# Optimization experiments

Measured on AMD Instinct MI355X. Metric: run time of the kernel, lower is better.

## Reference

```python
import jax, jax.numpy as jnp
import numpy as np

B, S, HID = 2, 2048, 2048
H, KV, D = 16, 4, 128          # query heads, kv heads, head_dim
G = H // KV                     # q heads per kv head
RD = 32                         # rotary_dim = int(0.25 * 128), even
THETA = 5000000.0
EPS = 1e-6


def _rms_norm(x, w):
    # out = x * rsqrt(mean(x^2)) * (1 + w)   (weight is zero-init)
    out = x * jax.lax.rsqrt(jnp.mean(x * x, axis=-1, keepdims=True) + EPS)
    return out * (1.0 + w.astype(x.dtype))


def _apply_rope(x, positions):
    # x: [B,S,h,RD]; standard HF rope with rotate_half on the rotary slice
    half = RD // 2
    inv_freq = 1.0 / (THETA ** (jnp.arange(0, half, dtype=jnp.float32) * 2.0 / RD))
    freqs = positions.astype(jnp.float32)[..., None] * inv_freq  # [B,S,half]
    emb = jnp.concatenate([freqs, freqs], axis=-1)               # [B,S,RD]
    cos = jnp.cos(emb)[:, :, None, :].astype(x.dtype)
    sin = jnp.sin(emb)[:, :, None, :].astype(x.dtype)
    x1, x2 = x[..., :half], x[..., half:]
    rot = jnp.concatenate([-x2, x1], axis=-1)
    return x * cos + rot * sin


def _partial_rope(q, k, positions):
    q_rot, q_pass = q[..., :RD], q[..., RD:]
    k_rot, k_pass = k[..., :RD], k[..., RD:]
    q_rot = _apply_rope(q_rot, positions)
    k_rot = _apply_rope(k_rot, positions)
    return (jnp.concatenate([q_rot, q_pass], axis=-1),
            jnp.concatenate([k_rot, k_pass], axis=-1))


def setup_inputs() -> dict:
    k0, k1, k2 = jax.random.split(jax.random.key(0), 3)
    x = jax.random.normal(k0, (B, S, HID), dtype=jnp.float32)
    positions = jnp.broadcast_to(jnp.arange(S, dtype=jnp.int32), (B, S))
    attention_mask = jnp.ones((B, S), dtype=bool)
    wqkv = jax.random.normal(k1, (HID, (H * 2 + 2 * KV) * D), dtype=jnp.float32) * 0.02
    wo = jax.random.normal(k2, (H * D, HID), dtype=jnp.float32) * 0.02
    q_norm_w = jnp.zeros((D,), dtype=jnp.float32)
    k_norm_w = jnp.zeros((D,), dtype=jnp.float32)
    return {"x": x, "positions": positions, "attention_mask": attention_mask,
            "wqkv": wqkv, "wo": wo, "q_norm_w": q_norm_w, "k_norm_w": k_norm_w}


def reference(x, positions, attention_mask, wqkv, wo, q_norm_w, k_norm_w):
    bsz, seq, _ = x.shape
    qkv = jnp.einsum('bsh,hf->bsf', x, wqkv)  # [B,S,5120]
    q_sz, kv_sz = H * 2 * D, KV * D
    q_raw = qkv[..., :q_sz]
    k_raw = qkv[..., q_sz:q_sz + kv_sz]
    v_raw = qkv[..., q_sz + kv_sz:]

    q_all = q_raw.reshape(bsz, seq, H, 2 * D)
    q, gate = jnp.split(q_all, 2, axis=-1)          # each [B,S,H,D]
    gate = gate.reshape(bsz, seq, H * D)

    q = _rms_norm(q, q_norm_w)
    k = _rms_norm(k_raw.reshape(bsz, seq, KV, D), k_norm_w)
    v = v_raw.reshape(bsz, seq, KV, D)
    q, k = _partial_rope(q, k, positions)

    # GQA causal attention, scale = 1/sqrt(head_dim)
    qg = q.reshape(bsz, seq, KV, G, D)
    scores = jnp.einsum('bqkgd,bskd->bkgqs', qg, k) * (1.0 / np.sqrt(D))
    causal = jnp.tril(jnp.ones((seq, seq), dtype=bool))
    mask = causal[None, None, None] & attention_mask[:, None, None, None, :]
    scores = jnp.where(mask, scores, jnp.finfo(scores.dtype).min)
    probs = jax.nn.softmax(scores, axis=-1)
    attn = jnp.einsum('bkgqs,bskd->bqkgd', probs, v)
    attn = attn.reshape(bsz, seq, H * D)

    attn = attn * jax.nn.sigmoid(gate)
    return jnp.einsum('bsf,fh->bsh', attn, wo)
```

## Files before the change

### kernel.cpp

```cpp
#include <hip/hip_runtime.h>

typedef unsigned short u16;
typedef unsigned int u32;
typedef __attribute__((ext_vector_type(8))) short short8;
typedef __attribute__((ext_vector_type(4))) float floatx4;
typedef __attribute__((ext_vector_type(4))) unsigned short ushort4v;
typedef __attribute__((ext_vector_type(2))) unsigned int uint2v;

#define SEQ   2048
#define HIDD  2048
#define NQH   16
#define NKV   4
#define HDIM  128
#define QKV_N 5120
#define K_OFF 4096
#define V_OFF 4608
#define NTOK  4096
#define PSTR  40

__device__ __forceinline__ float b2f(u16 u) {
  u32 x = ((u32)u) << 16;
  return __builtin_bit_cast(float, x);
}
__device__ __forceinline__ u16 f2b(float f) {
  u32 x = __builtin_bit_cast(u32, f);
  u32 r = x + 0x7fffu + ((x >> 16) & 1u);
  return (u16)(r >> 16);
}
__device__ __forceinline__ u32 cvt_pk_bf16(float lo, float hi) {
  u32 r;
  asm("v_cvt_pk_bf16_f32 %0, %1, %2" : "=v"(r) : "v"(lo), "v"(hi));
  return r;
}
__device__ __forceinline__ short8 pack8(floatx4 a, floatx4 b) {
  short8 s;
#pragma unroll
  for (int j = 0; j < 4; j++) { s[j] = (short)f2b(a[j]); s[4 + j] = (short)f2b(b[j]); }
  return s;
}
__device__ __forceinline__ void async_copy16(const u16* g, u16* lds) {
  __builtin_amdgcn_global_load_lds((const __attribute__((address_space(1))) u32*)g,
                                   (__attribute__((address_space(3))) u32*)lds, 16, 0, 0);
}

__global__ __launch_bounds__(256) void cast_bf16(const float* __restrict__ in,
                                                 u16* __restrict__ out, int n8) {
  const int i = blockIdx.x * 256 + threadIdx.x;
  if (i < n8) {
    const floatx4 f0 = *(const floatx4*)(in + (size_t)i * 8);
    const floatx4 f1 = *(const floatx4*)(in + (size_t)i * 8 + 4);
    *(short8*)(out + (size_t)i * 8) = pack8(f0, f1);
  }
}

__global__ __launch_bounds__(256) void transpose_f32_bf16(const float* __restrict__ in,
                                                          u16* __restrict__ out,
                                                          int R, int C) {
  __shared__ float tile[64][65];
  const int bx = blockIdx.x * 64;
  const int by = blockIdx.y * 64;
  const int tid = threadIdx.x;
  const int lr  = tid >> 2;
  const int lc4 = tid & 3;
#pragma unroll
  for (int i = 0; i < 4; i++) {
    const int c4 = lc4 * 4 + i;
    *(floatx4*)&tile[lr][c4 * 4] =
        *(const floatx4*)&in[(size_t)(by + lr) * C + bx + c4 * 4];
  }
  __syncthreads();
#pragma unroll
  for (int i = 0; i < 2; i++) {
    const int c  = (tid >> 3) + i * 32;
    const int r0 = (tid & 7) * 8;
    short8 v;
#pragma unroll
    for (int k = 0; k < 8; k++) v[k] = (short)f2b(tile[r0 + k][c]);
    *(short8*)&out[(size_t)(bx + c) * R + by + r0] = v;
  }
}

__global__ __launch_bounds__(256) void pack_kv(const u16* __restrict__ qkv,
                                               u16* __restrict__ Kc,
                                               u16* __restrict__ Vp) {
  __shared__ u16 tile[32][136];
  const int t0 = blockIdx.x * 32;
  const int kv = blockIdx.y;
  const int tid = threadIdx.x;
  const int b  = t0 / SEQ;
  const int tl = t0 - b * SEQ;
  const int jt = tl >> 5;
  const size_t kvbase = (size_t)(b * NKV + kv) * SEQ * HDIM;

  const int row  = tid >> 3;
  const int part = tid & 7;
  const size_t qbase = (size_t)(t0 + row) * QKV_N;
  const short8 kv0 = *(const short8*)(qkv + qbase + K_OFF + kv * HDIM + part * 16);
  const short8 kv1 = *(const short8*)(qkv + qbase + K_OFF + kv * HDIM + part * 16 + 8);
  *(short8*)(Kc + kvbase + (size_t)(tl + row) * HDIM + part * 16)     = kv0;
  *(short8*)(Kc + kvbase + (size_t)(tl + row) * HDIM + part * 16 + 8) = kv1;
  const short8 vv0 = *(const short8*)(qkv + qbase + V_OFF + kv * HDIM + part * 16);
  const short8 vv1 = *(const short8*)(qkv + qbase + V_OFF + kv * HDIM + part * 16 + 8);
  *(short8*)&tile[row][part * 16]     = vv0;
  *(short8*)&tile[row][part * 16 + 8] = vv1;
  __syncthreads();
  const int d = tid >> 1;
  const int half = tid & 1;
  u16* vout = Vp + kvbase + (size_t)jt * HDIM * 32 + d * 32 + half * 16;
  short8 o0;
#pragma unroll
  for (int i = 0; i < 8; i++) o0[i] = (short)tile[half * 16 + i][d];
  short8 o1;
#pragma unroll
  for (int i = 0; i < 8; i++) o1[i] = (short)tile[half * 16 + 8 + i][d];
  *(short8*)(vout) = o0;
  *(short8*)(vout + 8) = o1;
}

template <bool C32>
__global__ __launch_bounds__(512, 2) void gemm_bt8(const u16* __restrict__ A,
                                                   const u16* __restrict__ Bt,
                                                   void* __restrict__ Cp,
                                                   int M, int N, int K, int ldc) {
  __shared__ __align__(16) u16 As[2][256 * 64];
  __shared__ __align__(16) u16 Bs[2][256 * 64];
  const int tid  = threadIdx.x;
  const int wave = tid >> 6;
  const int lane = tid & 63;
  const int lm   = lane & 15;
  const int lq   = lane >> 4;
  const int nwg = gridDim.x * gridDim.y;
  const int bid = blockIdx.y * gridDim.x + blockIdx.x;
  const int sbid = (bid & 7) * (nwg >> 3) + (bid >> 3);
  const int m0   = (sbid / gridDim.x) * 256;
  const int n0   = (sbid % gridDim.x) * 256;
  const int wr   = wave >> 2;
  const int wc   = wave & 3;
  const int NK   = K >> 6;

  const int r0 = wave * 16 + (lane >> 3);
  const int c0 = (((lane & 7) ^ (r0 & 7)) << 3);
  const int dls = wave * 1024;

  auto stageA = [&](int buf, int kt, int h) {
    const u16* g = A + (size_t)(m0 + h * 128 + r0) * K + kt * 64 + c0;
    async_copy16(g,                &As[buf][h * 8192 + dls]);
    async_copy16(g + (size_t)8 * K, &As[buf][h * 8192 + dls + 512]);
  };
  auto stageB = [&](int buf, int kt, int h) {
    const u16* g = Bt + (size_t)(n0 + h * 128 + r0) * K + kt * 64 + c0;
    async_copy16(g,                &Bs[buf][h * 8192 + dls]);
    async_copy16(g + (size_t)8 * K, &Bs[buf][h * 8192 + dls + 512]);
  };
  auto rdA = [&](int buf, int row, int ch) {
    return *(const short8*)&As[buf][row * 64 + ((ch ^ (row & 7)) << 3)];
  };
  auto rdB = [&](int buf, int row, int ch) {
    return *(const short8*)&Bs[buf][row * 64 + ((ch ^ (row & 7)) << 3)];
  };

  floatx4 acc[8][4] = {};
  short8 aF[4][2], bF[4][2];

  stageA(0, 0, 0); stageA(0, 0, 1);
  stageB(0, 0, 0); stageB(0, 0, 1);
  stageB(1, 1, 0); stageB(1, 1, 1);
  asm volatile("s_waitcnt vmcnt(4)" ::: "memory");
  __builtin_amdgcn_sched_barrier(0);
  __builtin_amdgcn_s_barrier();

  for (int j = 0; j < NK; ++j) {
    const int cur = j & 1;
#pragma unroll
    for (int m = 0; m < 4; ++m)
#pragma unroll
      for (int kk = 0; kk < 2; ++kk)
        aF[m][kk] = rdA(cur, wr * 128 + m * 16 + lm, kk * 4 + lq);
#pragma unroll
    for (int n = 0; n < 2; ++n)
#pragma unroll
      for (int kk = 0; kk < 2; ++kk)
        bF[n][kk] = rdB(cur, wc * 64 + n * 16 + lm, kk * 4 + lq);
    if (j + 1 < NK) stageA(cur ^ 1, j + 1, 0);
    asm volatile("s_waitcnt lgkmcnt(8)" ::: "memory");
    __builtin_amdgcn_s_barrier();
    asm volatile("s_waitcnt lgkmcnt(0)" ::: "memory");
    __builtin_amdgcn_sched_barrier(0);
    __builtin_amdgcn_s_setprio(1);
#pragma unroll
    for (int m = 0; m < 4; ++m)
#pragma unroll
      for (int n = 0; n < 2; ++n)
#pragma unroll
        for (int kk = 0; kk < 2; ++kk)
          acc[m][n] = __builtin_amdgcn_mfma_f32_16x16x32_bf16(aF[m][kk], bF[n][kk], acc[m][n], 0, 0, 0);
    __builtin_amdgcn_s_setprio(0);
    __builtin_amdgcn_s_barrier();
#pragma unroll
    for (int n = 0; n < 2; ++n)
#pragma unroll
      for (int kk = 0; kk < 2; ++kk)
        bF[2 + n][kk] = rdB(cur, wc * 64 + (2 + n) * 16 + lm, kk * 4 + lq);
    if (j + 1 < NK) stageA(cur ^ 1, j + 1, 1);
    __builtin_amdgcn_s_barrier();
    asm volatile("s_waitcnt lgkmcnt(0)" ::: "memory");
    __builtin_amdgcn_sched_barrier(0);
    __builtin_amdgcn_s_setprio(1);
#pragma unroll
    for (int m = 0; m < 4; ++m)
#pragma unroll
      for (int n = 0; n < 2; ++n)
#pragma unroll
        for (int kk = 0; kk < 2; ++kk)
          acc[m][2 + n] = __builtin_amdgcn_mfma_f32_16x16x32_bf16(aF[m][kk], bF[2 + n][kk], acc[m][2 + n], 0, 0, 0);
    __builtin_amdgcn_s_setprio(0);
    __builtin_amdgcn_s_barrier();
#pragma unroll
    for (int m = 0; m < 4; ++m)
#pragma unroll
      for (int kk = 0; kk < 2; ++kk)
        aF[m][kk] = rdA(cur, wr * 128 + 64 + m * 16 + lm, kk * 4 + lq);
    if (j + 2 < NK) stageB(cur, j + 2, 0);
    __builtin_amdgcn_s_barrier();
    asm volatile("s_waitcnt lgkmcnt(0)" ::: "memory");
    __builtin_amdgcn_sched_barrier(0);
    __builtin_amdgcn_s_setprio(1);
#pragma unroll
    for (int m = 0; m < 4; ++m)
#pragma unroll
      for (int n = 0; n < 2; ++n)
#pragma unroll
        for (int kk = 0; kk < 2; ++kk)
          acc[4 + m][n] = __builtin_amdgcn_mfma_f32_16x16x32_bf16(aF[m][kk], bF[n][kk], acc[4 + m][n], 0, 0, 0);
    __builtin_amdgcn_s_setprio(0);
    __builtin_amdgcn_s_barrier();
    if (j + 2 < NK) stageB(cur, j + 2, 1);
    __builtin_amdgcn_s_barrier();
    __builtin_amdgcn_s_setprio(1);
#pragma unroll
    for (int m = 0; m < 4; ++m)
#pragma unroll
      for (int n = 0; n < 2; ++n)
#pragma unroll
        for (int kk = 0; kk < 2; ++kk)
          acc[4 + m][2 + n] = __builtin_amdgcn_mfma_f32_16x16x32_bf16(aF[m][kk], bF[2 + n][kk], acc[4 + m][2 + n], 0, 0, 0);
    __builtin_amdgcn_s_setprio(0);
    if (j + 2 < NK) asm volatile("s_waitcnt vmcnt(4)" ::: "memory");
    else            asm volatile("s_waitcnt vmcnt(0)" ::: "memory");
    __builtin_amdgcn_sched_barrier(0);
    __builtin_amdgcn_s_barrier();
  }

#pragma unroll
  for (int mi = 0; mi < 8; ++mi)
#pragma unroll
    for (int ni = 0; ni < 4; ++ni)
#pragma unroll
      for (int r = 0; r < 4; ++r) {
        const int row = m0 + wr * 128 + mi * 16 + lq * 4 + r;
        const int col = n0 + wc * 64 + ni * 16 + lm;
        if (C32) ((float*)Cp)[(size_t)row * ldc + col] = acc[mi][ni][r];
        else     ((u16*)Cp)[(size_t)row * ldc + col] = f2b(acc[mi][ni][r]);
      }
}

template <bool C32>
__global__ __launch_bounds__(256) void gemm_bt128(const u16* __restrict__ A,
                                                  const u16* __restrict__ Bt,
                                                  void* __restrict__ Cp,
                                                  int M, int N, int K, int ldc) {
  __shared__ __align__(16) u16 As[128 * 32];
  __shared__ __align__(16) u16 Bs[128 * 32];
  const int tid  = threadIdx.x;
  const int wave = tid >> 6;
  const int lane = tid & 63;
  const int m0 = blockIdx.y * 128;
  const int n0 = blockIdx.x * 128;
  const int wr = wave >> 1, wc = wave & 1;
  const int lrow = lane >> 2;
  const int lcol = (lane & 3) * 8;
  const int lm = lane & 15;
  const int lq = lane >> 4;

  floatx4 acc[4][4] = {};

  for (int k0 = 0; k0 < K; k0 += 32) {
#pragma unroll
    for (int i = 0; i < 2; i++) {
      const int r = wave * 32 + i * 16;
      async_copy16(A  + (size_t)(m0 + r + lrow) * K + k0 + lcol, &As[r * 32]);
      async_copy16(Bt + (size_t)(n0 + r + lrow) * K + k0 + lcol, &Bs[r * 32]);
    }
    __syncthreads();
    short8 aF[4], bF[4];
#pragma unroll
    for (int mi = 0; mi < 4; mi++)
      aF[mi] = *(const short8*)&As[(wr * 64 + mi * 16 + lm) * 32 + lq * 8];
#pragma unroll
    for (int ni = 0; ni < 4; ni++)
      bF[ni] = *(const short8*)&Bs[(wc * 64 + ni * 16 + lm) * 32 + lq * 8];
#pragma unroll
    for (int mi = 0; mi < 4; mi++)
#pragma unroll
      for (int ni = 0; ni < 4; ni++)
        acc[mi][ni] = __builtin_amdgcn_mfma_f32_16x16x32_bf16(aF[mi], bF[ni], acc[mi][ni], 0, 0, 0);
    __syncthreads();
  }

#pragma unroll
  for (int mi = 0; mi < 4; mi++)
#pragma unroll
    for (int ni = 0; ni < 4; ni++)
#pragma unroll
      for (int r = 0; r < 4; r++) {
        const int row = m0 + wr * 64 + mi * 16 + lq * 4 + r;
        const int col = n0 + wc * 64 + ni * 16 + lm;
        if (C32) ((float*)Cp)[(size_t)row * ldc + col] = acc[mi][ni][r];
        else     ((u16*)Cp)[(size_t)row * ldc + col] = f2b(acc[mi][ni][r]);
      }
}

template <bool C32>
__global__ __launch_bounds__(512, 2) void gemm_n128(const u16* __restrict__ A,
                                                    const u16* __restrict__ Bt,
                                                    void* __restrict__ Cp,
                                                    int M, int N, int K, int ldc) {
  __shared__ __align__(16) u16 As[2][256 * 64];
  __shared__ __align__(16) u16 Bs[2][128 * 64];
  const int tid  = threadIdx.x;
  const int wave = tid >> 6;
  const int lane = tid & 63;
  const int lm   = lane & 15;
  const int lq   = lane >> 4;
  const int nwg = gridDim.x * gridDim.y;
  const int bid = blockIdx.y * gridDim.x + blockIdx.x;
  const int sbid = (bid & 7) * (nwg >> 3) + (bid >> 3);
  const int m0   = (sbid / gridDim.x) * 256;
  const int n0   = (sbid % gridDim.x) * 128;
  const int wr   = wave >> 1;
  const int wc   = wave & 1;
  const int NK   = K >> 6;

  auto stA = [&](int buf, int kt, int L) {
    const int cd  = L * 512 + wave * 64 + lane;
    const int row = cd >> 3;
    const int ch  = cd & 7;
    async_copy16(A + (size_t)(m0 + row) * K + kt * 64 + ((ch ^ (row & 7)) << 3),
                 &As[buf][(L * 512 + wave * 64) * 8]);
  };
  auto stB = [&](int buf, int kt, int L) {
    const int cd  = L * 512 + wave * 64 + lane;
    const int row = cd >> 3;
    const int ch  = cd & 7;
    async_copy16(Bt + (size_t)(n0 + row) * K + kt * 64 + ((ch ^ (row & 7)) << 3),
                 &Bs[buf][(L * 512 + wave * 64) * 8]);
  };
  auto rdA = [&](int buf, int row, int ch) {
    return *(const short8*)&As[buf][row * 64 + ((ch ^ (row & 7)) << 3)];
  };
  auto rdB = [&](int buf, int row, int ch) {
    return *(const short8*)&Bs[buf][row * 64 + ((ch ^ (row & 7)) << 3)];
  };

  floatx4 acc[4][4] = {};
  short8 aF[4][2], bF[4][2];

  stA(0, 0, 0); stA(0, 0, 1); stA(0, 0, 2); stA(0, 0, 3);
  stB(0, 0, 0); stB(0, 0, 1);
  stB(1, 1, 0); stB(1, 1, 1);
  asm volatile("s_waitcnt vmcnt(2)" ::: "memory");
  __builtin_amdgcn_sched_barrier(0);
  __builtin_amdgcn_s_barrier();

  for (int j = 0; j < NK; ++j) {
    const int cur = j & 1;
#pragma unroll
    for (int m = 0; m < 4; ++m)
#pragma unroll
      for (int kk = 0; kk < 2; ++kk)
        aF[m][kk] = rdA(cur, wr * 64 + m * 16 + lm, kk * 4 + lq);
#pragma unroll
    for (int n = 0; n < 4; ++n)
#pragma unroll
      for (int kk = 0; kk < 2; ++kk)
        bF[n][kk] = rdB(cur, wc * 64 + n * 16 + lm, kk * 4 + lq);
    if (j + 1 < NK) { stA(cur ^ 1, j + 1, 0); stA(cur ^ 1, j + 1, 1); }
    asm volatile("s_waitcnt lgkmcnt(8)" ::: "memory");
    __builtin_amdgcn_s_barrier();
    asm volatile("s_waitcnt lgkmcnt(0)" ::: "memory");
    __builtin_amdgcn_sched_barrier(0);
    __builtin_amdgcn_s_setprio(1);
#pragma unroll
    for (int m = 0; m < 4; ++m)
#pragma unroll
      for (int n = 0; n < 2; ++n)
#pragma unroll
        for (int kk = 0; kk < 2; ++kk)
          acc[m][n] = __builtin_amdgcn_mfma_f32_16x16x32_bf16(aF[m][kk], bF[n][kk], acc[m][n], 0, 0, 0);
    __builtin_amdgcn_s_setprio(0);
    __builtin_amdgcn_s_barrier();
    if (j + 1 < NK) { stA(cur ^ 1, j + 1, 2); stA(cur ^ 1, j + 1, 3); }
    if (j + 2 < NK) { stB(cur, j + 2, 0); stB(cur, j + 2, 1); }
    __builtin_amdgcn_s_barrier();
    __builtin_amdgcn_sched_barrier(0);
    __builtin_amdgcn_s_setprio(1);
#pragma unroll
    for (int m = 0; m < 4; ++m)
#pragma unroll
      for (int n = 0; n < 2; ++n)
#pragma unroll
        for (int kk = 0; kk < 2; ++kk)
          acc[m][2 + n] = __builtin_amdgcn_mfma_f32_16x16x32_bf16(aF[m][kk], bF[2 + n][kk], acc[m][2 + n], 0, 0, 0);
    __builtin_amdgcn_s_setprio(0);
    if (j + 2 < NK) asm volatile("s_waitcnt vmcnt(2)" ::: "memory");
    else            asm volatile("s_waitcnt vmcnt(0)" ::: "memory");
    __builtin_amdgcn_sched_barrier(0);
    __builtin_amdgcn_s_barrier();
  }

#pragma unroll
  for (int mi = 0; mi < 4; ++mi)
#pragma unroll
    for (int ni = 0; ni < 4; ++ni)
#pragma unroll
      for (int r = 0; r < 4; ++r) {
        const int row = m0 + wr * 64 + mi * 16 + lq * 4 + r;
        const int col = n0 + wc * 64 + ni * 16 + lm;
        if (C32) ((float*)Cp)[(size_t)row * ldc + col] = acc[mi][ni][r];
        else     ((u16*)Cp)[(size_t)row * ldc + col] = f2b(acc[mi][ni][r]);
      }
}

__global__ __launch_bounds__(256) void postproc(u16* __restrict__ qkv,
                                                const int* __restrict__ positions,
                                                const float* __restrict__ qw,
                                                const float* __restrict__ kw) {
  const int u    = blockIdx.y;
  const int wv   = threadIdx.x >> 6;
  const int lane = threadIdx.x & 63;
  const float* w;
  int base;
  if (u < NQH) { base = u * 256; w = qw; }
  else         { base = K_OFF + (u - NQH) * HDIM; w = kw; }
  const int d0 = lane * 2;
  const float w0 = 1.0f + w[d0];
  const float w1 = 1.0f + w[d0 + 1];
  float inv0 = 0.0f, inv1 = 0.0f;
  if (d0 < 32) {
    const int i = d0 & 15;
    inv0 = __powf(5.0e6f, -((float)i) / 16.0f);
    inv1 = __powf(5.0e6f, -((float)(i + 1)) / 16.0f);
  }
  const float qsc = (u < NQH) ? 0.08838834764831845f : 1.0f;
#pragma unroll
  for (int it = 0; it < 4; ++it) {
    const int tok = blockIdx.x * 16 + wv * 4 + it;
    u16* p = qkv + (size_t)tok * QKV_N + base;
    float v0 = b2f(p[d0]);
    float v1 = b2f(p[d0 + 1]);
    float ss = v0 * v0 + v1 * v1;
#pragma unroll
    for (int off = 32; off >= 1; off >>= 1) ss += __shfl_xor(ss, off, 64);
    const float rs = rsqrtf(ss * (1.0f / 128.0f) + 1e-6f);
    v0 = v0 * rs * w0;
    v1 = v1 * rs * w1;
    const float pv0 = __shfl_xor(v0, 8, 64);
    const float pv1 = __shfl_xor(v1, 8, 64);
    if (d0 < 32) {
      const float fpos = (float)positions[tok];
      float s0, c0, s1, c1;
      __sincosf(fpos * inv0, &s0, &c0);
      __sincosf(fpos * inv1, &s1, &c1);
      if (d0 < 16) { v0 = v0 * c0 - pv0 * s0; v1 = v1 * c1 - pv1 * s1; }
      else         { v0 = v0 * c0 + pv0 * s0; v1 = v1 * c1 + pv1 * s1; }
    }
    p[d0]     = f2b(v0 * qsc);
    p[d0 + 1] = f2b(v1 * qsc);
  }
}

__global__ __launch_bounds__(256) void attn_kernel(const u16* __restrict__ qkv,
                                                   const u16* __restrict__ Kc,
                                                   const u16* __restrict__ Vp,
                                                   u16* __restrict__ attn_g) {
  __shared__ __align__(16) u16 Ks[2][4][32][32];
  __shared__ __align__(16) u16 Vs[2][128][32];
  __shared__ __align__(16) u16 P_lds[4][16 * PSTR];
  const int tid  = threadIdx.x;
  const int wave = tid >> 6;
  const int lane = tid & 63;
  const int lm = lane & 15;
  const int lq = lane >> 4;
  const int bx   = blockIdx.x;
  const int pair = bx & 7;
  const int kvi  = pair & 3;
  const int b    = pair >> 2;
  const int u    = bx >> 3;
  const int kk_  = u >> 5;
  const int cc_  = u & 31;
  const int t    = (kk_ == 0) ? 127 - cc_ : (kk_ == 1) ? 64 + cc_
                 : (kk_ == 2) ? 63 - cc_  : cc_;
  const int h   = kvi * 4 + wave;
  const size_t tokbase = (size_t)b * SEQ;
  const size_t kvbase  = (size_t)(b * NKV + kvi) * SEQ * HDIM;
  const int klocal = lane >> 2;
  const int ssw = ((lane & 3) ^ ((lane >> 3) & 3)) * 8;
  const int rsw = (lq ^ ((lm >> 1) & 3)) * 8;

  short8 onesF;
#pragma unroll
  for (int j = 0; j < 8; j++) onesF[j] = (short)0x3F80;

  auto stage = [&](int buf, int j) {
    const u16* ksrc = Kc + kvbase + (size_t)j * 32 * HDIM;
#pragma unroll
    for (int half = 0; half < 2; half++)
      async_copy16(ksrc + (size_t)(half * 16 + klocal) * HDIM + wave * 32 + ssw,
                   &Ks[buf][wave][half * 16][0]);
    const u16* vsrc = Vp + kvbase + (size_t)j * (HDIM * 32);
#pragma unroll
    for (int i = 0; i < 2; i++)
      async_copy16(vsrc + wave * 1024 + i * 512 + (lane >> 2) * 32 + ssw,
                   &Vs[buf][wave * 32 + i * 16][0]);
  };

  short8 qF[4];
  const u16* qp = qkv + (tokbase + 16 * t + lm) * QKV_N + h * 256;
#pragma unroll
  for (int kc = 0; kc < 4; kc++)
    qF[kc] = *(const short8*)(qp + kc * 32 + lq * 8);

  floatx4 O[8] = {};
  floatx4 lacc = {};
  const int jmax = t >> 1;
  const int moff = (t & 1) * 16;

  stage(0, 0);
  for (int j = 0; j <= jmax; j++) {
    const int cur = j & 1;
    __syncthreads();
    if (j < jmax) stage(cur ^ 1, j + 1);
    short8 kF[2][4], vF[8];
#pragma unroll
    for (int n0 = 0; n0 < 2; n0++)
#pragma unroll
      for (int kc = 0; kc < 4; kc++)
        kF[n0][kc] = *(const short8*)&Ks[cur][kc][n0 * 16 + lm][rsw];
#pragma unroll
    for (int dc = 0; dc < 8; dc++)
      vF[dc] = *(const short8*)&Vs[cur][dc * 16 + lm][rsw];

    floatx4 Sc[2] = {};
#pragma unroll
    for (int n0 = 0; n0 < 2; n0++)
#pragma unroll
      for (int kc = 0; kc < 4; kc++)
        Sc[n0] = __builtin_amdgcn_mfma_f32_16x16x32_bf16(kF[n0][kc], qF[kc], Sc[n0], 0, 0, 0);

    const bool masked = (j == jmax);
    u32 pk[4];
#pragma unroll
    for (int n0 = 0; n0 < 2; n0++) {
      float pe[4];
#pragma unroll
      for (int r = 0; r < 4; r++) {
        float e = __expf(Sc[n0][r]);
        if (masked) {
          const int keyloc = n0 * 16 + lq * 4 + r;
          e = (keyloc <= lm + moff) ? e : 0.0f;
        }
        pe[r] = e;
      }
      pk[n0 * 2]     = cvt_pk_bf16(pe[0], pe[1]);
      pk[n0 * 2 + 1] = cvt_pk_bf16(pe[2], pe[3]);
    }
    {
      uint2v w0; w0.x = pk[0]; w0.y = pk[1];
      uint2v w1; w1.x = pk[2]; w1.y = pk[3];
      *(uint2v*)&P_lds[wave][lm * PSTR + lq * 4]      = w0;
      *(uint2v*)&P_lds[wave][lm * PSTR + 16 + lq * 4] = w1;
    }
    __builtin_amdgcn_sched_barrier(0);
    const short8 pF = *(const short8*)&P_lds[wave][lm * PSTR + lq * 8];
    lacc = __builtin_amdgcn_mfma_f32_16x16x32_bf16(onesF, pF, lacc, 0, 0, 0);
#pragma unroll
    for (int dc = 0; dc < 8; dc++)
      O[dc] = __builtin_amdgcn_mfma_f32_16x16x32_bf16(vF[dc], pF, O[dc], 0, 0, 0);
  }

  {
    const float inv_l = 1.0f / lacc[0];
    const size_t tok = tokbase + 16 * t + lm;
    const u16* gp = qkv + tok * QKV_N + h * 256 + 128 + lq * 4;
    u16* op = attn_g + tok * HIDD + h * HDIM + lq * 4;
#pragma unroll
    for (int dc = 0; dc < 8; dc++) {
      const ushort4v gv = *(const ushort4v*)(gp + dc * 16);
      float ov[4];
#pragma unroll
      for (int r = 0; r < 4; r++) {
        const float g = b2f(gv[r]);
        const float sg = 1.0f / (1.0f + __expf(-g));
        ov[r] = O[dc][r] * inv_l * sg;
      }
      uint2v st;
      st.x = cvt_pk_bf16(ov[0], ov[1]);
      st.y = cvt_pk_bf16(ov[2], ov[3]);
      *(uint2v*)(op + dc * 16) = st;
    }
  }
}

extern "C" void kernel_launch(void* const* d_in, const int* in_sizes, int n_in,
                              void* d_out, int out_size, void* d_ws, size_t ws_size,
                              hipStream_t stream) {
  const float* x        = (const float*)d_in[0];
  const int* positions  = (const int*)d_in[1];
  const float* wqkv     = (const float*)d_in[3];
  const float* wo       = (const float*)d_in[4];
  const float* qnw      = (const float*)d_in[5];
  const float* knw      = (const float*)d_in[6];
  float* out = (float*)d_out;

  char* ws = (char*)d_ws;
  u16* qkv    = (u16*)(ws);
  u16* wqkv_t = (u16*)(ws + 41943040);
  u16* attn_g = (u16*)(ws + 41943040);
  u16* Kc     = (u16*)(ws + 58720256);
  u16* wo_t   = (u16*)(ws);
  u16* xb     = (u16*)d_out;
  u16* Vp     = (u16*)d_out;

  cast_bf16<<<dim3(NTOK * HIDD / 8 / 256), 256, 0, stream>>>(x, xb, NTOK * HIDD / 8);
  transpose_f32_bf16<<<dim3(QKV_N / 64, HIDD / 64), 256, 0, stream>>>(wqkv, wqkv_t, HIDD, QKV_N);
  gemm_bt8<false><<<dim3(4096 / 256, NTOK / 256), 512, 0, stream>>>(
      xb, wqkv_t, qkv, NTOK, 4096, HIDD, QKV_N);
  gemm_bt128<false><<<dim3(1024 / 128, NTOK / 128), 256, 0, stream>>>(
      xb, wqkv_t + (size_t)4096 * HIDD, qkv + 4096, NTOK, 1024, HIDD, QKV_N);
  postproc<<<dim3(NTOK / 16, NQH + NKV), 256, 0, stream>>>(qkv, positions, qnw, knw);
  pack_kv<<<dim3(NTOK / 32, NKV), 256, 0, stream>>>(qkv, Kc, Vp);
  attn_kernel<<<dim3(1024), 256, 0, stream>>>(qkv, Kc, Vp, attn_g);
  transpose_f32_bf16<<<dim3(HIDD / 64, HIDD / 64), 256, 0, stream>>>(wo, wo_t, HIDD, HIDD);
  gemm_n128<true><<<dim3(HIDD / 128, NTOK / 256), 512, 0, stream>>>(
      attn_g, wo_t, out, NTOK, HIDD, HIDD, HIDD);
}
```

Baseline: 370.2 us.

## Process two 16-row query subtiles per wave to reuse staged K/V tiles

Each attention block now covers 32 query rows per head (two 16-row subtiles) and iterates over the shared K/V tiles once for both. The grid is halved to 512 blocks. This cuts K/V staging loads and LDS fragment reads per query and amortizes the loop overhead. In exchange it doubles the accumulator registers, which may reduce occupancy, and it adds an explicit LDS wait between the two P write/read phases.

Measured after the change: 385.9 us. 1.04x slower.

```diff
diff --git a/kernel.cpp b/kernel.cpp
--- a/kernel.cpp
+++ b/kernel.cpp
@@ -485,7 +485,7 @@
                                                    u16* __restrict__ attn_g) {
   __shared__ __align__(16) u16 Ks[2][4][32][32];
   __shared__ __align__(16) u16 Vs[2][128][32];
-  __shared__ __align__(16) u16 P_lds[4][16 * PSTR];
+  __shared__ __align__(16) u16 P_lds[4][2][16 * PSTR];
   const int tid  = threadIdx.x;
   const int wave = tid >> 6;
   const int lane = tid & 63;
@@ -496,10 +496,8 @@
   const int kvi  = pair & 3;
   const int b    = pair >> 2;
   const int u    = bx >> 3;
-  const int kk_  = u >> 5;
   const int cc_  = u & 31;
-  const int t    = (kk_ == 0) ? 127 - cc_ : (kk_ == 1) ? 64 + cc_
-                 : (kk_ == 2) ? 63 - cc_  : cc_;
+  const int T    = (u >> 5) ? cc_ : 63 - cc_;
   const int h   = kvi * 4 + wave;
   const size_t tokbase = (size_t)b * SEQ;
   const size_t kvbase  = (size_t)(b * NKV + kvi) * SEQ * HDIM;
@@ -524,16 +522,18 @@
                    &Vs[buf][wave * 32 + i * 16][0]);
   };
 
-  short8 qF[4];
-  const u16* qp = qkv + (tokbase + 16 * t + lm) * QKV_N + h * 256;
-#pragma unroll
-  for (int kc = 0; kc < 4; kc++)
-    qF[kc] = *(const short8*)(qp + kc * 32 + lq * 8);
-
-  floatx4 O[8] = {};
-  floatx4 lacc = {};
-  const int jmax = t >> 1;
-  const int moff = (t & 1) * 16;
+  short8 qF[2][4];
+#pragma unroll
+  for (int s = 0; s < 2; s++) {
+    const u16* qp = qkv + (tokbase + 32 * T + s * 16 + lm) * QKV_N + h * 256;
+#pragma unroll
+    for (int kc = 0; kc < 4; kc++)
+      qF[s][kc] = *(const short8*)(qp + kc * 32 + lq * 8);
+  }
+
+  floatx4 O[2][8] = {};
+  floatx4 lacc[2] = {};
+  const int jmax = T;
 
   stage(0, 0);
   for (int j = 0; j <= jmax; j++) {
@@ -550,47 +550,53 @@
     for (int dc = 0; dc < 8; dc++)
       vF[dc] = *(const short8*)&Vs[cur][dc * 16 + lm][rsw];
 
-    floatx4 Sc[2] = {};
-#pragma unroll
-    for (int n0 = 0; n0 < 2; n0++)
-#pragma unroll
-      for (int kc = 0; kc < 4; kc++)
-        Sc[n0] = __builtin_amdgcn_mfma_f32_16x16x32_bf16(kF[n0][kc], qF[kc], Sc[n0], 0, 0, 0);
-
     const bool masked = (j == jmax);
-    u32 pk[4];
-#pragma unroll
-    for (int n0 = 0; n0 < 2; n0++) {
-      float pe[4];
-#pragma unroll
-      for (int r = 0; r < 4; r++) {
-        float e = __expf(Sc[n0][r]);
-        if (masked) {
-          const int keyloc = n0 * 16 + lq * 4 + r;
-          e = (keyloc <= lm + moff) ? e : 0.0f;
+#pragma unroll
+    for (int s = 0; s < 2; s++) {
+      floatx4 Sc[2] = {};
+#pragma unroll
+      for (int n0 = 0; n0 < 2; n0++)
+#pragma unroll
+        for (int kc = 0; kc < 4; kc++)
+          Sc[n0] = __builtin_amdgcn_mfma_f32_16x16x32_bf16(kF[n0][kc], qF[s][kc], Sc[n0], 0, 0, 0);
+
+      u32 pk[4];
+#pragma unroll
+      for (int n0 = 0; n0 < 2; n0++) {
+        float pe[4];
+#pragma unroll
+        for (int r = 0; r < 4; r++) {
+          float e = __expf(Sc[n0][r]);
+          if (masked) {
+            const int keyloc = n0 * 16 + lq * 4 + r;
+            e = (keyloc <= lm + s * 16) ? e : 0.0f;
+          }
+          pe[r] = e;
         }
-        pe[r] = e;
+        pk[n0 * 2]     = cvt_pk_bf16(pe[0], pe[1]);
+        pk[n0 * 2 + 1] = cvt_pk_bf16(pe[2], pe[3]);
       }
-      pk[n0 * 2]     = cvt_pk_bf16(pe[0], pe[1]);
-      pk[n0 * 2 + 1] = cvt_pk_bf16(pe[2], pe[3]);
+      {
+        uint2v w0; w0.x = pk[0]; w0.y = pk[1];
+        uint2v w1; w1.x = pk[2]; w1.y = pk[3];
+        *(uint2v*)&P_lds[wave][s][lm * PSTR + lq * 4]      = w0;
+        *(uint2v*)&P_lds[wave][s][lm * PSTR + 16 + lq * 4] = w1;
+      }
+      __builtin_amdgcn_sched_barrier(0);
+      asm volatile("s_waitcnt lgkmcnt(0)" ::: "memory");
+      __builtin_amdgcn_sched_barrier(0);
+      const short8 pF = *(const short8*)&P_lds[wave][s][lm * PSTR + lq * 8];
+      lacc[s] = __builtin_amdgcn_mfma_f32_16x16x32_bf16(onesF, pF, lacc[s], 0, 0, 0);
+#pragma unroll
+      for (int dc = 0; dc < 8; dc++)
+        O[s][dc] = __builtin_amdgcn_mfma_f32_16x16x32_bf16(vF[dc], pF, O[s][dc], 0, 0, 0);
     }
-    {
-      uint2v w0; w0.x = pk[0]; w0.y = pk[1];
-      uint2v w1; w1.x = pk[2]; w1.y = pk[3];
-      *(uint2v*)&P_lds[wave][lm * PSTR + lq * 4]      = w0;
-      *(uint2v*)&P_lds[wave][lm * PSTR + 16 + lq * 4] = w1;
-    }
-    __builtin_amdgcn_sched_barrier(0);
-    const short8 pF = *(const short8*)&P_lds[wave][lm * PSTR + lq * 8];
-    lacc = __builtin_amdgcn_mfma_f32_16x16x32_bf16(onesF, pF, lacc, 0, 0, 0);
-#pragma unroll
-    for (int dc = 0; dc < 8; dc++)
-      O[dc] = __builtin_amdgcn_mfma_f32_16x16x32_bf16(vF[dc], pF, O[dc], 0, 0, 0);
-  }
-
-  {
-    const float inv_l = 1.0f / lacc[0];
-    const size_t tok = tokbase + 16 * t + lm;
+  }
+
+#pragma unroll
+  for (int s = 0; s < 2; s++) {
+    const float inv_l = 1.0f / lacc[s][0];
+    const size_t tok = tokbase + 32 * T + s * 16 + lm;
     const u16* gp = qkv + tok * QKV_N + h * 256 + 128 + lq * 4;
     u16* op = attn_g + tok * HIDD + h * HDIM + lq * 4;
 #pragma unroll
@@ -601,7 +607,7 @@
       for (int r = 0; r < 4; r++) {
         const float g = b2f(gv[r]);
         const float sg = 1.0f / (1.0f + __expf(-g));
-        ov[r] = O[dc][r] * inv_l * sg;
+        ov[r] = O[s][dc][r] * inv_l * sg;
       }
       uint2v st;
       st.x = cvt_pk_bf16(ov[0], ov[1]);
@@ -639,7 +645,7 @@
       xb, wqkv_t + (size_t)4096 * HIDD, qkv + 4096, NTOK, 1024, HIDD, QKV_N);
   postproc<<<dim3(NTOK / 16, NQH + NKV), 256, 0, stream>>>(qkv, positions, qnw, knw);
   pack_kv<<<dim3(NTOK / 32, NKV), 256, 0, stream>>>(qkv, Kc, Vp);
-  attn_kernel<<<dim3(1024), 256, 0, stream>>>(qkv, Kc, Vp, attn_g);
+  attn_kernel<<<dim3(512), 256, 0, stream>>>(qkv, Kc, Vp, attn_g);
   transpose_f32_bf16<<<dim3(HIDD / 64, HIDD / 64), 256, 0, stream>>>(wo, wo_t, HIDD, HIDD);
   gemm_n128<true><<<dim3(HIDD / 128, NTOK / 256), 512, 0, stream>>>(
       attn_g, wo_t, out, NTOK, HIDD, HIDD, HIDD);
```
